# Optimization experiments

Hardware: AMD Instinct MI355X
Metric: run time of the kernel (lower is better)

Reference implementation:

```python
import jax, jax.numpy as jnp
import numpy as np

H = 8          # n_heads
DK = 128       # d_model // h
D = H * DK     # d_model = 1024
B, S = 8, 1024
D_LIST = (32, 64, 96, 128)  # sorted set of hidden//h from config dict


def setup_inputs() -> dict:
    key = jax.random.key(0)
    ks = jax.random.split(key, 13)
    mk = lambda k, shape: jax.random.normal(k, shape, dtype=jnp.float32)
    inp = {
        'query': mk(ks[0], (B, S, D)),
        'key': mk(ks[1], (B, S, D)),
        'value': mk(ks[2], (B, S, D)),
        'config_idx': jax.random.randint(ks[3], (B,), 0, len(D_LIST), dtype=jnp.int32),
        'Wq': mk(ks[4], (D, D)) * 0.02, 'bq': jnp.zeros((D,), jnp.float32),
        'Wk': mk(ks[5], (D, D)) * 0.02, 'bk': jnp.zeros((D,), jnp.float32),
        'Wv': mk(ks[6], (D, D)) * 0.02, 'bv': jnp.zeros((D,), jnp.float32),
        'Wo': mk(ks[7], (D, D)) * 0.02, 'bo': jnp.zeros((D,), jnp.float32),
    }
    return inp


def _mha_arrange(query, key, value, config_idx, Wq, bq, Wk, bk, Wv, bv, Wo, bo):
    Bb, Ss, _ = query.shape
    proj = lambda x, W, b: (x @ W.T + b).reshape(Bb, Ss, H, DK).transpose(0, 2, 1, 3)
    q = proj(query, Wq, bq)   # [B,H,S,DK]
    k = proj(key, Wk, bk)
    v = proj(value, Wv, bv)
    scores = jnp.einsum('bhqd,bhkd->bhqk', q, k) / np.float32(np.sqrt(DK))
    p = jax.nn.softmax(scores, axis=-1)
    ctx = jnp.einsum('bhqk,bhkd->bhqd', p, v).transpose(0, 2, 1, 3)  # [B,S,H,DK]
    # attn_arrange: per-sample width d; pack first d dims of each head densely
    ret = jnp.zeros((Bb, Ss, H * DK), query.dtype)
    for i, d in enumerate(D_LIST):
        packed = ctx[:, :, :, :d].reshape(Bb, Ss, H * d)           # [B,S,H*d]
        packed = jnp.pad(packed, ((0, 0), (0, 0), (0, H * (DK - d))))
        sel = (config_idx == i)[:, None, None]
        ret = ret + jnp.where(sel, packed, jnp.zeros((), query.dtype))
    return ret @ Wo.T + bo


def reference(query, key, value, config_idx, Wq, bq, Wk, bk, Wv, bv, Wo, bo):
    return _mha_arrange(query, key, value, config_idx, Wq, bq, Wk, bk, Wv, bv, Wo, bo)
```

## Files before the change

kernel.cpp:

```cpp
#include <hip/hip_runtime.h>
#include <hip/hip_bf16.h>


typedef __attribute__((ext_vector_type(8))) __bf16 bf16x8;
typedef __attribute__((ext_vector_type(4))) float f32x4;

#define DEV static __device__ __forceinline__

DEV float exp2v(float x) { return __builtin_amdgcn_exp2f(x); }

DEV unsigned short f2bf(float f) {
  union { float f; unsigned int u; } c; c.f = f;
  unsigned int u = c.u + 0x7fffu + ((c.u >> 16) & 1u);
  return (unsigned short)(u >> 16);
}

DEV unsigned cvtpk(float a, float b) {
  unsigned r;
  asm("v_cvt_pk_bf16_f32 %0, %1, %2" : "=v"(r) : "v"(a), "v"(b));
  return r;
}

DEV void gload16(const void* g, void* l) {
  __builtin_amdgcn_global_load_lds((const __attribute__((address_space(1))) void*)g,
                                   (__attribute__((address_space(3))) void*)l, 16, 0, 0);
}

#define LGKM0 do { asm volatile("s_waitcnt lgkmcnt(0)" ::: "memory"); \
                   __builtin_amdgcn_sched_barrier(0); } while (0)
#define BAR   __builtin_amdgcn_s_barrier()
#define VMC4  asm volatile("s_waitcnt vmcnt(4)" ::: "memory")
#define VMC0  asm volatile("s_waitcnt vmcnt(0)" ::: "memory")

DEV void cv4(const float* __restrict__ s, unsigned short* __restrict__ d, int i) {
  const float4 a = *(const float4*)(s + i);
  ushort4 o;
  o.x = f2bf(a.x); o.y = f2bf(a.y); o.z = f2bf(a.z); o.w = f2bf(a.w);
  *(ushort4*)(d + i) = o;
}

__global__ __launch_bounds__(256) void convert_kernel(
    const float* __restrict__ q, const float* __restrict__ k, const float* __restrict__ v,
    const float* __restrict__ wq, const float* __restrict__ wk,
    const float* __restrict__ wv, const float* __restrict__ wo,
    unsigned short* __restrict__ xq, unsigned short* __restrict__ xk,
    unsigned short* __restrict__ xv, unsigned short* __restrict__ wb)
{
  const int i = (blockIdx.x * 256 + threadIdx.x) * 4;
  cv4(q, xq, i);
  cv4(k, xk, i);
  cv4(v, xv, i);
  if (i < 4 * 1024 * 1024) {
    const int which = i >> 20, off = i & 1048575;
    const float* s = which == 0 ? wq : which == 1 ? wk : which == 2 ? wv : wo;
    cv4(s, wb + (which << 20), off);
  }
}

template<int OUTMODE>
__global__ __launch_bounds__(512, 2) void gemm8p(
    const unsigned short* __restrict__ xq, const unsigned short* __restrict__ xk,
    const unsigned short* __restrict__ xv, const unsigned short* __restrict__ wb,
    const float* __restrict__ bq, const float* __restrict__ bk,
    const float* __restrict__ bv,
    unsigned short* __restrict__ Qp, unsigned short* __restrict__ Kp,
    unsigned short* __restrict__ VTp, float* __restrict__ fout)
{
  __shared__ __align__(16) char LDS[131072];
  int z, mt, nt;
  if (OUTMODE == 0) {
    const int swz = ((blockIdx.x & 7) * 48) + (blockIdx.x >> 3);
    z = swz >> 7; const int rem = swz & 127; mt = rem >> 2; nt = rem & 3;
  } else {
    const int swz = ((blockIdx.x & 7) * 16) + (blockIdx.x >> 3);
    z = 0; mt = swz >> 2; nt = swz & 3;
  }
  const int m0 = mt * 256, n0 = nt * 256;
  const unsigned short* Ag = (OUTMODE == 1) ? xq : (z == 0 ? xq : z == 1 ? xk : xv);
  const unsigned short* Bg = (OUTMODE == 1) ? wb : wb + ((size_t)z << 20);
  const float* bias = (OUTMODE == 1) ? bq : (z == 0 ? bq : z == 1 ? bk : bv);

  const int tid = threadIdx.x, lane = tid & 63, w = tid >> 6;
  const int wm = w >> 2, wn = w & 3;
  const int g = lane >> 4, ln = lane & 15;

  const f32x4 fzero = {0.f, 0.f, 0.f, 0.f};
  f32x4 acc[8][4];
#pragma unroll
  for (int i = 0; i < 8; i++)
#pragma unroll
    for (int j = 0; j < 4; j++) acc[i][j] = fzero;

  bf16x8 bfr[4][2];
  bf16x8 afr[2][2];

  auto stageA = [&](int bf, int hf, int k0) {
    const unsigned short* src = Ag + (size_t)(m0 + hf * 128) * 1024 + k0;
    char* base = LDS + bf * 32768 + hf * 16384 + w * 2048;
#pragma unroll
    for (int r2 = 0; r2 < 2; ++r2) {
      const int o = w * 2048 + r2 * 1024 + lane * 16;
      const int rwi = o >> 7, cb = o & 127;
      gload16(src + (size_t)rwi * 1024 + ((cb ^ ((rwi & 7) << 4)) >> 1), base + r2 * 1024);
    }
  };
  auto stageB = [&](int bf, int hf, int k0) {
    const unsigned short* src = Bg + (size_t)(n0 + hf * 128) * 1024 + k0;
    char* base = LDS + 65536 + bf * 32768 + hf * 16384 + w * 2048;
#pragma unroll
    for (int r2 = 0; r2 < 2; ++r2) {
      const int o = w * 2048 + r2 * 1024 + lane * 16;
      const int rwi = o >> 7, cb = o & 127;
      gload16(src + (size_t)rwi * 1024 + ((cb ^ ((rwi & 7) << 4)) >> 1), base + r2 * 1024);
    }
  };
  auto rdA = [&](int bf, int q) {
#pragma unroll
    for (int p = 0; p < 2; ++p)
#pragma unroll
      for (int kc = 0; kc < 2; ++kc) {
        const int rwi = (2 * q + p) * 16 + ln;
        const int cb = (kc * 64 + g * 16) ^ ((rwi & 7) << 4);
        afr[p][kc] = *(const bf16x8*)(LDS + bf * 32768 + wm * 16384 + rwi * 128 + cb);
      }
  };
  auto rdB = [&](int bf) {
#pragma unroll
    for (int nf = 0; nf < 4; ++nf)
#pragma unroll
      for (int kc = 0; kc < 2; ++kc) {
        const int rwi = (wn & 1) * 64 + nf * 16 + ln;
        const int cb = (kc * 64 + g * 16) ^ ((rwi & 7) << 4);
        bfr[nf][kc] = *(const bf16x8*)(LDS + 65536 + bf * 32768 + (wn >> 1) * 16384 + rwi * 128 + cb);
      }
  };
  auto mm = [&](int q) {
    __builtin_amdgcn_s_setprio(1);
#pragma unroll
    for (int p = 0; p < 2; ++p)
#pragma unroll
      for (int nf = 0; nf < 4; ++nf)
#pragma unroll
        for (int kc = 0; kc < 2; ++kc)
          acc[2 * q + p][nf] =
              __builtin_amdgcn_mfma_f32_16x16x32_bf16(afr[p][kc], bfr[nf][kc],
                                                      acc[2 * q + p][nf], 0, 0, 0);
    __builtin_amdgcn_s_setprio(0);
  };

  stageB(0, 0, 0); stageB(0, 1, 0);
  stageA(0, 0, 0); stageA(0, 1, 0);
  stageB(1, 0, 64); stageB(1, 1, 64);
  VMC4; BAR;

  for (int j = 0; j < 8; ++j) {
    const int kO = (2 * j + 1) << 6, kNE = (2 * j + 2) << 6, kNO = (2 * j + 3) << 6;
    const bool pf = j < 7;
    rdB(0); rdA(0, 0); stageA(1, 0, kO);
    LGKM0; BAR; mm(0); BAR;
    rdA(0, 1); stageA(1, 1, kO);
    LGKM0; BAR; mm(1); BAR;
    rdA(0, 2); if (pf) stageB(0, 0, kNE);
    LGKM0; BAR; mm(2); BAR;
    rdA(0, 3); if (pf) stageB(0, 1, kNE);
    LGKM0; BAR; mm(3);
    if (pf) { VMC4; } else { VMC0; }
    BAR;
    rdB(1); rdA(1, 0); if (pf) stageA(0, 0, kNE);
    LGKM0; BAR; mm(0); BAR;
    rdA(1, 1); if (pf) stageA(0, 1, kNE);
    LGKM0; BAR; mm(1); BAR;
    rdA(1, 2); if (pf) stageB(1, 0, kNO);
    LGKM0; BAR; mm(2); BAR;
    rdA(1, 3); if (pf) stageB(1, 1, kNO);
    LGKM0; BAR; mm(3);
    if (pf) { VMC4; }
    BAR;
  }

  const float QS = 0.12751743f;
#pragma unroll
  for (int mf = 0; mf < 8; ++mf)
#pragma unroll
    for (int nf = 0; nf < 4; ++nf) {
      const int m = m0 + wm * 128 + mf * 16 + g * 4;
      const int n = n0 + wn * 64 + nf * 16 + ln;
      const float bn = bias[n];
      if (OUTMODE == 1) {
#pragma unroll
        for (int r = 0; r < 4; ++r)
          fout[(size_t)(m + r) * 1024 + n] = acc[mf][nf][r] + bn;
      } else if (z == 0) {
#pragma unroll
        for (int r = 0; r < 4; ++r)
          Qp[(size_t)(m + r) * 1024 + n] = f2bf((acc[mf][nf][r] + bn) * QS);
      } else if (z == 1) {
#pragma unroll
        for (int r = 0; r < 4; ++r)
          Kp[(size_t)(m + r) * 1024 + n] = f2bf(acc[mf][nf][r] + bn);
      } else {
        const int b = m >> 10, s0 = m & 1023;
        uint2 pk;
        pk.x = cvtpk(acc[mf][nf][0] + bn, acc[mf][nf][1] + bn);
        pk.y = cvtpk(acc[mf][nf][2] + bn, acc[mf][nf][3] + bn);
        *(uint2*)(VTp + (((size_t)(b * 8) << 7 | n) << 10) + s0) = pk;
      }
    }
}

__global__ __launch_bounds__(256) void attn_kernel(
    const unsigned short* __restrict__ Qp, const unsigned short* __restrict__ Kp,
    const unsigned short* __restrict__ VT, const int* __restrict__ cfg,
    unsigned short* __restrict__ ret)
{
  __shared__ __align__(16) unsigned short Ks[2][64 * 128];
  __shared__ __align__(16) unsigned short Vs[2][128 * 64];
  __shared__ __align__(16) unsigned short Ps[4 * 16 * 64];
  const int bx = blockIdx.x;
  const int qb = bx >> 6, bh = bx & 63, b = bh >> 3, h = bh & 7;
  const int tid = threadIdx.x, lane = tid & 63, w = tid >> 6;
  const int g = lane >> 4, ln = lane & 15;
  const int q0 = qb * 64;
  const f32x4 fzero = {0.f, 0.f, 0.f, 0.f};

  bf16x8 qf[4];
  {
    const unsigned short* qrow = Qp + ((size_t)(b * 1024 + q0 + w * 16 + ln)) * 1024 + h * 128;
#pragma unroll
    for (int kc = 0; kc < 4; kc++) qf[kc] = *(const bf16x8*)(qrow + kc * 32 + g * 8);
  }
  float m_run = -1e30f, l_run = 0.f;
  f32x4 o_acc[8];
#pragma unroll
  for (int i = 0; i < 8; i++) o_acc[i] = fzero;

  auto stage = [&](int buf, int kv0) {
#pragma unroll
    for (int i = 0; i < 4; ++i) {
      const int obase = i * 4096 + w * 1024;
      const int o = obase + lane * 16;
      {
        const int r = o >> 8, cb = o & 255;
        const int cs = cb ^ ((r & 7) << 4);
        gload16(Kp + ((size_t)(b * 1024 + kv0 + r)) * 1024 + h * 128 + (cs >> 1),
                (char*)Ks + buf * 16384 + obase);
      }
      {
        const int r = o >> 7, cb = o & 127;
        const int cs = cb ^ ((r & 7) << 4);
        gload16(VT + ((size_t)((b * 8 + h) * 128 + r)) * 1024 + kv0 + (cs >> 1),
                (char*)Vs + buf * 16384 + obase);
      }
    }
  };

  stage(0, 0);
  asm volatile("s_waitcnt vmcnt(0)" ::: "memory");
  __syncthreads();

  int cur = 0;
  for (int t = 0; t < 16; ++t) {
    if (t < 15) stage(cur ^ 1, (t + 1) * 64);

    f32x4 sc[4];
    __builtin_amdgcn_s_setprio(1);
#pragma unroll
    for (int nb = 0; nb < 4; ++nb) {
      sc[nb] = fzero;
      const int rr = nb * 16 + ln;
      const int sw = (rr & 7) << 4;
#pragma unroll
      for (int kc = 0; kc < 4; ++kc) {
        const bf16x8 kf = *(const bf16x8*)((const char*)Ks + cur * 16384 + rr * 256 +
                                           (((kc * 32 + g * 8) << 1) ^ sw));
        sc[nb] = __builtin_amdgcn_mfma_f32_16x16x32_bf16(kf, qf[kc], sc[nb], 0, 0, 0);
      }
    }
    __builtin_amdgcn_s_setprio(0);

    float mnb[4];
#pragma unroll
    for (int nb = 0; nb < 4; ++nb)
      mnb[nb] = fmaxf(fmaxf(sc[nb][0], sc[nb][1]), fmaxf(sc[nb][2], sc[nb][3]));
    float pmax = fmaxf(fmaxf(mnb[0], mnb[1]), fmaxf(mnb[2], mnb[3]));
    pmax = fmaxf(pmax, __shfl_xor(pmax, 16));
    pmax = fmaxf(pmax, __shfl_xor(pmax, 32));
    if (__any(pmax > m_run + 11.5f)) {
      const float mnew = fmaxf(m_run, pmax);
      const float alpha = exp2v(m_run - mnew);
      l_run *= alpha;
      m_run = mnew;
      float ar[4];
#pragma unroll
      for (int r = 0; r < 4; ++r)
        ar[r] = __shfl(alpha, (lane & 48) | (((lane >> 4) & 3) << 2) | r);
#pragma unroll
      for (int i = 0; i < 8; i++)
#pragma unroll
        for (int r = 0; r < 4; r++) o_acc[i][r] *= ar[r];
    }
    float sum = 0.f;
    float pvv[16];
#pragma unroll
    for (int nb = 0; nb < 4; ++nb)
#pragma unroll
      for (int r = 0; r < 4; ++r) {
        const float p = exp2v(sc[nb][r] - m_run);
        pvv[nb * 4 + r] = p; sum += p;
      }
    l_run += sum;

    {
      char* pbase = (char*)Ps + w * 2048 + ln * 128;
#pragma unroll
      for (int nb = 0; nb < 4; ++nb) {
        uint2 pk;
        pk.x = cvtpk(pvv[nb * 4 + 0], pvv[nb * 4 + 1]);
        pk.y = cvtpk(pvv[nb * 4 + 2], pvv[nb * 4 + 3]);
        *(uint2*)(pbase + (((16 * nb + 4 * g) << 1) ^ ((ln & 7) << 4))) = pk;
      }
    }
    bf16x8 pf[2];
#pragma unroll
    for (int kc = 0; kc < 2; kc++)
      pf[kc] = *(const bf16x8*)((const char*)Ps + w * 2048 + ln * 128 +
                                (((kc * 32 + g * 8) << 1) ^ ((ln & 7) << 4)));

    __builtin_amdgcn_s_setprio(1);
#pragma unroll
    for (int nb2 = 0; nb2 < 8; ++nb2) {
      const int rr = nb2 * 16 + ln;
      const int sw = (rr & 7) << 4;
#pragma unroll
      for (int kc = 0; kc < 2; ++kc) {
        const bf16x8 vf = *(const bf16x8*)((const char*)Vs + cur * 16384 + rr * 128 +
                                           (((kc * 32 + g * 8) << 1) ^ sw));
        o_acc[nb2] = __builtin_amdgcn_mfma_f32_16x16x32_bf16(pf[kc], vf, o_acc[nb2], 0, 0, 0);
      }
    }
    __builtin_amdgcn_s_setprio(0);

    if (t < 15) {
      asm volatile("s_waitcnt vmcnt(0)" ::: "memory");
      __syncthreads();
    }
    cur ^= 1;
  }

  l_run += __shfl_xor(l_run, 16);
  l_run += __shfl_xor(l_run, 32);
  float rl[4];
#pragma unroll
  for (int r = 0; r < 4; ++r)
    rl[r] = 1.0f / __shfl(l_run, (lane & 48) | (((lane >> 4) & 3) << 2) | r);
  const int d_b = 32 * (cfg[b] + 1);
  const int zw = 128 - d_b;
  const size_t rowbase = (size_t)(b * 1024 + q0 + w * 16 + g * 4);
#pragma unroll
  for (int nb2 = 0; nb2 < 8; ++nb2) {
    const int dk = nb2 * 16 + ln;
    if (dk < d_b) {
#pragma unroll
      for (int r = 0; r < 4; r++)
        ret[(rowbase + r) * 1024 + h * d_b + dk] = f2bf(o_acc[nb2][r] * rl[r]);
    } else {
#pragma unroll
      for (int r = 0; r < 4; r++)
        ret[(rowbase + r) * 1024 + 8 * d_b + h * zw + (dk - d_b)] = 0;
    }
  }
}

extern "C" void kernel_launch(void* const* d_in, const int* in_sizes, int n_in,
                              void* d_out, int out_size, void* d_ws, size_t ws_size,
                              hipStream_t stream)
{
  (void)in_sizes; (void)n_in; (void)out_size; (void)ws_size;
  const float* q   = (const float*)d_in[0];
  const float* k   = (const float*)d_in[1];
  const float* v   = (const float*)d_in[2];
  const int*   cfg = (const int*)d_in[3];
  const float* Wq  = (const float*)d_in[4];  const float* bq = (const float*)d_in[5];
  const float* Wk  = (const float*)d_in[6];  const float* bk = (const float*)d_in[7];
  const float* Wv  = (const float*)d_in[8];  const float* bv = (const float*)d_in[9];
  const float* Wo  = (const float*)d_in[10]; const float* bo = (const float*)d_in[11];

  const size_t X  = 8192ull * 1024ull;
  const size_t WN = 1024ull * 1024ull;
  char* p = (char*)d_ws;
  unsigned short* xq  = (unsigned short*)p; p += X * 2;
  unsigned short* xk  = (unsigned short*)p; p += X * 2;
  unsigned short* xv  = (unsigned short*)p; p += X * 2;
  unsigned short* wb  = (unsigned short*)p; p += 4 * WN * 2;
  unsigned short* Qp  = (unsigned short*)p; p += X * 2;
  unsigned short* Kp  = (unsigned short*)p; p += X * 2;
  unsigned short* VTp = (unsigned short*)p; p += X * 2;
  unsigned short* ret = (unsigned short*)p; p += X * 2;

  convert_kernel<<<dim3(8192), dim3(256), 0, stream>>>(q, k, v, Wq, Wk, Wv, Wo,
                                                       xq, xk, xv, wb);

  gemm8p<0><<<dim3(384), dim3(512), 0, stream>>>(xq, xk, xv, wb, bq, bk, bv,
                                                 Qp, Kp, VTp, nullptr);

  attn_kernel<<<dim3(1024), dim3(256), 0, stream>>>(Qp, Kp, VTp, cfg, ret);

  gemm8p<1><<<dim3(128), dim3(512), 0, stream>>>(ret, nullptr, nullptr, wb + 3 * WN,
                                                 bo, nullptr, nullptr,
                                                 nullptr, nullptr, nullptr,
                                                 (float*)d_out);
}
```

Baseline: 194.7 us.

## Fuse fp32-to-bf16 activation conversion into QKV GEMM A-tile staging

The separate conversion pass for query/key/value is removed. The QKV GEMM now loads fp32 A tiles into registers, converts them with packed bf16 conversion and writes them to LDS, while weights are still pre-converted. This avoids writing and rereading three bf16 activation copies. The GEMM tile also shrinks from 256x256 to 256x128 with a triple-buffered pipeline and twice as many blocks, at the cost of more register pressure and fp32 global read traffic inside the GEMM.

```diff
diff --git a/kernel.cpp b/kernel.cpp
--- a/kernel.cpp
+++ b/kernel.cpp
@@ -29,8 +29,7 @@
 #define LGKM0 do { asm volatile("s_waitcnt lgkmcnt(0)" ::: "memory"); \
                    __builtin_amdgcn_sched_barrier(0); } while (0)
 #define BAR   __builtin_amdgcn_s_barrier()
-#define VMC4  asm volatile("s_waitcnt vmcnt(4)" ::: "memory")
-#define VMC0  asm volatile("s_waitcnt vmcnt(0)" ::: "memory")
+#define VMC(n) asm volatile("s_waitcnt vmcnt(" #n ")" ::: "memory")
 
 DEV void cv4(const float* __restrict__ s, unsigned short* __restrict__ d, int i) {
   const float4 a = *(const float4*)(s + i);
@@ -39,100 +38,114 @@
   *(ushort4*)(d + i) = o;
 }
 
-__global__ __launch_bounds__(256) void convert_kernel(
-    const float* __restrict__ q, const float* __restrict__ k, const float* __restrict__ v,
+__global__ __launch_bounds__(256) void convert_w(
     const float* __restrict__ wq, const float* __restrict__ wk,
     const float* __restrict__ wv, const float* __restrict__ wo,
-    unsigned short* __restrict__ xq, unsigned short* __restrict__ xk,
-    unsigned short* __restrict__ xv, unsigned short* __restrict__ wb)
+    unsigned short* __restrict__ wb)
 {
   const int i = (blockIdx.x * 256 + threadIdx.x) * 4;
-  cv4(q, xq, i);
-  cv4(k, xk, i);
-  cv4(v, xv, i);
-  if (i < 4 * 1024 * 1024) {
-    const int which = i >> 20, off = i & 1048575;
-    const float* s = which == 0 ? wq : which == 1 ? wk : which == 2 ? wv : wo;
-    cv4(s, wb + (which << 20), off);
-  }
-}
-
-template<int OUTMODE>
-__global__ __launch_bounds__(512, 2) void gemm8p(
-    const unsigned short* __restrict__ xq, const unsigned short* __restrict__ xk,
-    const unsigned short* __restrict__ xv, const unsigned short* __restrict__ wb,
+  const int which = i >> 20, off = i & 1048575;
+  const float* s = which == 0 ? wq : which == 1 ? wk : which == 2 ? wv : wo;
+  cv4(s, wb + (which << 20), off);
+}
+
+template<int AMODE>
+__global__ __launch_bounds__(512, 2) void gemm3b(
+    const float* __restrict__ Aq, const float* __restrict__ Ak,
+    const float* __restrict__ Av, const unsigned short* __restrict__ Abf,
+    const unsigned short* __restrict__ wbase,
     const float* __restrict__ bq, const float* __restrict__ bk,
     const float* __restrict__ bv,
     unsigned short* __restrict__ Qp, unsigned short* __restrict__ Kp,
     unsigned short* __restrict__ VTp, float* __restrict__ fout)
 {
-  __shared__ __align__(16) char LDS[131072];
+  __shared__ __align__(16) char LDS[147456];
   int z, mt, nt;
-  if (OUTMODE == 0) {
-    const int swz = ((blockIdx.x & 7) * 48) + (blockIdx.x >> 3);
-    z = swz >> 7; const int rem = swz & 127; mt = rem >> 2; nt = rem & 3;
+  if (AMODE == 0) {
+    const int swz = (blockIdx.x & 7) * 96 + (blockIdx.x >> 3);
+    z = swz >> 8; const int rem = swz & 255; mt = rem >> 3; nt = rem & 7;
   } else {
-    const int swz = ((blockIdx.x & 7) * 16) + (blockIdx.x >> 3);
-    z = 0; mt = swz >> 2; nt = swz & 3;
-  }
-  const int m0 = mt * 256, n0 = nt * 256;
-  const unsigned short* Ag = (OUTMODE == 1) ? xq : (z == 0 ? xq : z == 1 ? xk : xv);
-  const unsigned short* Bg = (OUTMODE == 1) ? wb : wb + ((size_t)z << 20);
-  const float* bias = (OUTMODE == 1) ? bq : (z == 0 ? bq : z == 1 ? bk : bv);
+    const int swz = (blockIdx.x & 7) * 32 + (blockIdx.x >> 3);
+    z = 0; mt = swz >> 3; nt = swz & 7;
+  }
+  const int m0 = mt * 256, n0 = nt * 128;
+  const float* Af = (AMODE == 0) ? (z == 0 ? Aq : z == 1 ? Ak : Av) : nullptr;
+  const unsigned short* Bg = wbase + ((size_t)(AMODE == 0 ? z : 0) << 20);
+  const float* bias = (AMODE == 0) ? (z == 0 ? bq : z == 1 ? bk : bv) : bq;
 
   const int tid = threadIdx.x, lane = tid & 63, w = tid >> 6;
-  const int wm = w >> 2, wn = w & 3;
+  const int wm = w >> 1, wn = w & 1;
   const int g = lane >> 4, ln = lane & 15;
 
   const f32x4 fzero = {0.f, 0.f, 0.f, 0.f};
-  f32x4 acc[8][4];
-#pragma unroll
-  for (int i = 0; i < 8; i++)
+  f32x4 acc[4][4];
+#pragma unroll
+  for (int i = 0; i < 4; i++)
 #pragma unroll
     for (int j = 0; j < 4; j++) acc[i][j] = fzero;
 
-  bf16x8 bfr[4][2];
-  bf16x8 afr[2][2];
-
-  auto stageA = [&](int bf, int hf, int k0) {
-    const unsigned short* src = Ag + (size_t)(m0 + hf * 128) * 1024 + k0;
-    char* base = LDS + bf * 32768 + hf * 16384 + w * 2048;
-#pragma unroll
-    for (int r2 = 0; r2 < 2; ++r2) {
-      const int o = w * 2048 + r2 * 1024 + lane * 16;
-      const int rwi = o >> 7, cb = o & 127;
-      gload16(src + (size_t)rwi * 1024 + ((cb ^ ((rwi & 7) << 4)) >> 1), base + r2 * 1024);
-    }
-  };
-  auto stageB = [&](int bf, int hf, int k0) {
-    const unsigned short* src = Bg + (size_t)(n0 + hf * 128) * 1024 + k0;
-    char* base = LDS + 65536 + bf * 32768 + hf * 16384 + w * 2048;
-#pragma unroll
-    for (int r2 = 0; r2 < 2; ++r2) {
-      const int o = w * 2048 + r2 * 1024 + lane * 16;
-      const int rwi = o >> 7, cb = o & 127;
-      gload16(src + (size_t)rwi * 1024 + ((cb ^ ((rwi & 7) << 4)) >> 1), base + r2 * 1024);
-    }
-  };
-  auto rdA = [&](int bf, int q) {
-#pragma unroll
-    for (int p = 0; p < 2; ++p)
-#pragma unroll
-      for (int kc = 0; kc < 2; ++kc) {
-        const int rwi = (2 * q + p) * 16 + ln;
-        const int cb = (kc * 64 + g * 16) ^ ((rwi & 7) << 4);
-        afr[p][kc] = *(const bf16x8*)(LDS + bf * 32768 + wm * 16384 + rwi * 128 + cb);
-      }
-  };
-  auto rdB = [&](int bf) {
-#pragma unroll
-    for (int nf = 0; nf < 4; ++nf)
-#pragma unroll
-      for (int kc = 0; kc < 2; ++kc) {
-        const int rwi = (wn & 1) * 64 + nf * 16 + ln;
-        const int cb = (kc * 64 + g * 16) ^ ((rwi & 7) << 4);
-        bfr[nf][kc] = *(const bf16x8*)(LDS + 65536 + bf * 32768 + (wn >> 1) * 16384 + rwi * 128 + cb);
-      }
+  bf16x8 afr[2][2], bfr[4][2];
+
+  auto SB = [&](int buf, int k0) {
+    char* base = LDS + 98304 + buf * 16384 + w * 2048;
+#pragma unroll
+    for (int j2 = 0; j2 < 2; ++j2) {
+      const int o = w * 2048 + j2 * 1024 + lane * 16;
+      const int row = o >> 7, cb = o & 127;
+      gload16(Bg + (size_t)(n0 + row) * 1024 + k0 + ((cb ^ ((row & 7) << 4)) >> 1),
+              base + j2 * 1024);
+    }
+  };
+  auto SA = [&](int buf, int hf, int k0) {
+    char* base = LDS + buf * 32768 + hf * 16384 + w * 2048;
+#pragma unroll
+    for (int j2 = 0; j2 < 2; ++j2) {
+      const int o = w * 2048 + j2 * 1024 + lane * 16;
+      const int row = o >> 7, cb = o & 127;
+      gload16(Abf + (size_t)(m0 + hf * 128 + row) * 1024 + k0 + ((cb ^ ((row & 7) << 4)) >> 1),
+              base + j2 * 1024);
+    }
+  };
+
+  const int arow = tid >> 2;
+  const int acol = (tid & 3) << 4;
+  const int wsw = (arow & 7) << 4;
+  const int wc0 = ((tid & 3) * 32) ^ wsw;
+  const int wc1 = ((tid & 3) * 32 + 16) ^ wsw;
+
+#define LA4(d0, d1, d2, d3, hf, k0) do { \
+    const float* _s = Af + (size_t)(m0 + (hf) * 128 + arow) * 1024 + (k0) + acol; \
+    d0 = *(const float4*)(_s); d1 = *(const float4*)(_s + 4); \
+    d2 = *(const float4*)(_s + 8); d3 = *(const float4*)(_s + 12); } while (0)
+
+#define WA4(buf, hf, s0, s1, s2, s3) do { \
+    char* _d = LDS + (buf) * 32768 + (hf) * 16384 + arow * 128; \
+    uint4 _p0, _p1; \
+    _p0.x = cvtpk(s0.x, s0.y); _p0.y = cvtpk(s0.z, s0.w); \
+    _p0.z = cvtpk(s1.x, s1.y); _p0.w = cvtpk(s1.z, s1.w); \
+    _p1.x = cvtpk(s2.x, s2.y); _p1.y = cvtpk(s2.z, s2.w); \
+    _p1.z = cvtpk(s3.x, s3.y); _p1.w = cvtpk(s3.z, s3.w); \
+    *(uint4*)(_d + wc0) = _p0; *(uint4*)(_d + wc1) = _p1; } while (0)
+
+  auto rdA = [&](int buf, int q) {
+#pragma unroll
+    for (int p = 0; p < 2; ++p) {
+      const int row = wm * 64 + (2 * q + p) * 16 + ln;
+      const int sw = (row & 7) << 4;
+#pragma unroll
+      for (int kc = 0; kc < 2; ++kc)
+        afr[p][kc] = *(const bf16x8*)(LDS + buf * 32768 + row * 128 + ((kc * 64 + g * 16) ^ sw));
+    }
+  };
+  auto rdB = [&](int buf) {
+#pragma unroll
+    for (int nf = 0; nf < 4; ++nf) {
+      const int row = wn * 64 + nf * 16 + ln;
+      const int sw = (row & 7) << 4;
+#pragma unroll
+      for (int kc = 0; kc < 2; ++kc)
+        bfr[nf][kc] = *(const bf16x8*)(LDS + 98304 + buf * 16384 + row * 128 + ((kc * 64 + g * 16) ^ sw));
+    }
   };
   auto mm = [&](int q) {
     __builtin_amdgcn_s_setprio(1);
@@ -148,62 +161,95 @@
     __builtin_amdgcn_s_setprio(0);
   };
 
-  stageB(0, 0, 0); stageB(0, 1, 0);
-  stageA(0, 0, 0); stageA(0, 1, 0);
-  stageB(1, 0, 64); stageB(1, 1, 64);
-  VMC4; BAR;
-
-  for (int j = 0; j < 8; ++j) {
-    const int kO = (2 * j + 1) << 6, kNE = (2 * j + 2) << 6, kNO = (2 * j + 3) << 6;
-    const bool pf = j < 7;
-    rdB(0); rdA(0, 0); stageA(1, 0, kO);
-    LGKM0; BAR; mm(0); BAR;
-    rdA(0, 1); stageA(1, 1, kO);
-    LGKM0; BAR; mm(1); BAR;
-    rdA(0, 2); if (pf) stageB(0, 0, kNE);
-    LGKM0; BAR; mm(2); BAR;
-    rdA(0, 3); if (pf) stageB(0, 1, kNE);
-    LGKM0; BAR; mm(3);
-    if (pf) { VMC4; } else { VMC0; }
-    BAR;
-    rdB(1); rdA(1, 0); if (pf) stageA(0, 0, kNE);
-    LGKM0; BAR; mm(0); BAR;
-    rdA(1, 1); if (pf) stageA(0, 1, kNE);
-    LGKM0; BAR; mm(1); BAR;
-    rdA(1, 2); if (pf) stageB(1, 0, kNO);
-    LGKM0; BAR; mm(2); BAR;
-    rdA(1, 3); if (pf) stageB(1, 1, kNO);
-    LGKM0; BAR; mm(3);
-    if (pf) { VMC4; }
-    BAR;
-  }
+  float4 a00, a01, a02, a03, a04, a05, a06, a07;
+  float4 a10, a11, a12, a13, a14, a15, a16, a17;
+
+  if (AMODE == 0) {
+    LA4(a00, a01, a02, a03, 0, 0);
+    LA4(a04, a05, a06, a07, 1, 0);
+    SB(0, 0);
+    LA4(a10, a11, a12, a13, 0, 64);
+    LA4(a14, a15, a16, a17, 1, 64);
+    SB(1, 64);
+    WA4(0, 0, a00, a01, a02, a03);
+    WA4(0, 1, a04, a05, a06, a07);
+    VMC(10);
+  } else {
+    SA(0, 0, 0); SA(0, 1, 0);
+    SB(0, 0);
+    SA(1, 0, 64); SA(1, 1, 64);
+    SB(1, 64);
+    VMC(6);
+  }
+  LGKM0; BAR;
+
+#define TILE(t, L0, L1, L2, L3, L4, L5, L6, L7, W0, W1, W2, W3, W4, W5, W6, W7, br, bn, bw) \
+  do { \
+    const int _kL = ((t) + 2) << 6; \
+    const bool _ld = (t) < 14, _wr = (t) < 15; \
+     \
+    rdB(br); rdA(br, 0); \
+    if (AMODE == 0) { \
+      if (_ld) LA4(L0, L1, L2, L3, 0, _kL); \
+      if (_wr) WA4(bn, 0, W0, W1, W2, W3); \
+    } else { \
+      if (_ld) SA(bw, 0, _kL); \
+    } \
+    BAR; LGKM0; mm(0); BAR; \
+     \
+    rdA(br, 1); \
+    if (AMODE == 0) { \
+      if (_ld) LA4(L4, L5, L6, L7, 1, _kL); \
+      if (_wr) WA4(bn, 1, W4, W5, W6, W7); \
+    } else { \
+      if (_ld) SA(bw, 1, _kL); \
+    } \
+    if (_ld) SB(bw, _kL); \
+    BAR; LGKM0; mm(1); \
+    if (_ld) { if (AMODE == 0) VMC(10); else VMC(6); } \
+    else if ((t) < 15) VMC(0); \
+    BAR; \
+  } while (0)
+
+  int br = 0, bn = 1, bw = 2;
+  for (int t2 = 0; t2 < 16; t2 += 2) {
+    TILE(t2, a00, a01, a02, a03, a04, a05, a06, a07,
+             a10, a11, a12, a13, a14, a15, a16, a17, br, bn, bw);
+    { const int x = br; br = bn; bn = bw; bw = x; }
+    TILE(t2 + 1, a10, a11, a12, a13, a14, a15, a16, a17,
+                 a00, a01, a02, a03, a04, a05, a06, a07, br, bn, bw);
+    { const int x = br; br = bn; bn = bw; bw = x; }
+  }
+#undef TILE
+#undef LA4
+#undef WA4
 
   const float QS = 0.12751743f;
 #pragma unroll
-  for (int mf = 0; mf < 8; ++mf)
+  for (int mf = 0; mf < 4; ++mf)
 #pragma unroll
     for (int nf = 0; nf < 4; ++nf) {
-      const int m = m0 + wm * 128 + mf * 16 + g * 4;
+      const int m = m0 + wm * 64 + mf * 16 + g * 4;
       const int n = n0 + wn * 64 + nf * 16 + ln;
-      const float bn = bias[n];
-      if (OUTMODE == 1) {
+      const float bn_ = bias[n];
+      if (AMODE == 1) {
 #pragma unroll
         for (int r = 0; r < 4; ++r)
-          fout[(size_t)(m + r) * 1024 + n] = acc[mf][nf][r] + bn;
+          fout[(size_t)(m + r) * 1024 + n] = acc[mf][nf][r] + bn_;
       } else if (z == 0) {
 #pragma unroll
         for (int r = 0; r < 4; ++r)
-          Qp[(size_t)(m + r) * 1024 + n] = f2bf((acc[mf][nf][r] + bn) * QS);
+          Qp[(size_t)(m + r) * 1024 + n] = f2bf((acc[mf][nf][r] + bn_) * QS);
       } else if (z == 1) {
 #pragma unroll
         for (int r = 0; r < 4; ++r)
-          Kp[(size_t)(m + r) * 1024 + n] = f2bf(acc[mf][nf][r] + bn);
+          Kp[(size_t)(m + r) * 1024 + n] = f2bf(acc[mf][nf][r] + bn_);
       } else {
         const int b = m >> 10, s0 = m & 1023;
         uint2 pk;
-        pk.x = cvtpk(acc[mf][nf][0] + bn, acc[mf][nf][1] + bn);
-        pk.y = cvtpk(acc[mf][nf][2] + bn, acc[mf][nf][3] + bn);
-        *(uint2*)(VTp + (((size_t)(b * 8) << 7 | n) << 10) + s0) = pk;
+        pk.x = cvtpk(acc[mf][nf][0] + bn_, acc[mf][nf][1] + bn_);
+        pk.y = cvtpk(acc[mf][nf][2] + bn_, acc[mf][nf][3] + bn_);
+        *(uint2*)(VTp + (((size_t)(b * 1024 + n)) << 10) + s0) = pk;
       }
     }
 }
@@ -388,25 +434,21 @@
   const size_t X  = 8192ull * 1024ull;
   const size_t WN = 1024ull * 1024ull;
   char* p = (char*)d_ws;
-  unsigned short* xq  = (unsigned short*)p; p += X * 2;
-  unsigned short* xk  = (unsigned short*)p; p += X * 2;
-  unsigned short* xv  = (unsigned short*)p; p += X * 2;
   unsigned short* wb  = (unsigned short*)p; p += 4 * WN * 2;
   unsigned short* Qp  = (unsigned short*)p; p += X * 2;
   unsigned short* Kp  = (unsigned short*)p; p += X * 2;
   unsigned short* VTp = (unsigned short*)p; p += X * 2;
   unsigned short* ret = (unsigned short*)p; p += X * 2;
 
-  convert_kernel<<<dim3(8192), dim3(256), 0, stream>>>(q, k, v, Wq, Wk, Wv, Wo,
-                                                       xq, xk, xv, wb);
-
-  gemm8p<0><<<dim3(384), dim3(512), 0, stream>>>(xq, xk, xv, wb, bq, bk, bv,
-                                                 Qp, Kp, VTp, nullptr);
+  convert_w<<<dim3(4096), dim3(256), 0, stream>>>(Wq, Wk, Wv, Wo, wb);
+
+  gemm3b<0><<<dim3(768), dim3(512), 0, stream>>>(q, k, v, nullptr, wb,
+                                                 bq, bk, bv, Qp, Kp, VTp, nullptr);
 
   attn_kernel<<<dim3(1024), dim3(256), 0, stream>>>(Qp, Kp, VTp, cfg, ret);
 
-  gemm8p<1><<<dim3(128), dim3(512), 0, stream>>>(ret, nullptr, nullptr, wb + 3 * WN,
-                                                 bo, nullptr, nullptr,
+  gemm3b<1><<<dim3(256), dim3(512), 0, stream>>>(nullptr, nullptr, nullptr, ret,
+                                                 wb + 3 * WN, bo, nullptr, nullptr,
                                                  nullptr, nullptr, nullptr,
                                                  (float*)d_out);
 }
```

Result: slower. 203.5 us (+4.5%).

## Replace output projection with smaller-tile GEMM and reorder barriers in QKV GEMM

Applied to the files above, without the earlier changes.

The output projection previously reused the 256x256-tile pipelined GEMM with only 128 blocks, which underfills a chip with many CUs. A new simple 128x128-tile kernel launches 512 blocks of 256 threads to raise parallelism, at the cost of no software pipelining (synchronous load then compute each k-step). The QKV GEMM's LDS wait macro drops its sched_barrier, and the wait now sits after the workgroup barrier, which gives the compiler more freedom to schedule the LDS reads against the MFMAs.

```diff
diff --git a/kernel.cpp b/kernel.cpp
--- a/kernel.cpp
+++ b/kernel.cpp
@@ -26,8 +26,7 @@
                                    (__attribute__((address_space(3))) void*)l, 16, 0, 0);
 }
 
-#define LGKM0 do { asm volatile("s_waitcnt lgkmcnt(0)" ::: "memory"); \
-                   __builtin_amdgcn_sched_barrier(0); } while (0)
+#define LGKM0 asm volatile("s_waitcnt lgkmcnt(0)" ::: "memory")
 #define BAR   __builtin_amdgcn_s_barrier()
 #define VMC4  asm volatile("s_waitcnt vmcnt(4)" ::: "memory")
 #define VMC0  asm volatile("s_waitcnt vmcnt(0)" ::: "memory")
@@ -57,28 +56,22 @@
   }
 }
 
-template<int OUTMODE>
 __global__ __launch_bounds__(512, 2) void gemm8p(
     const unsigned short* __restrict__ xq, const unsigned short* __restrict__ xk,
     const unsigned short* __restrict__ xv, const unsigned short* __restrict__ wb,
     const float* __restrict__ bq, const float* __restrict__ bk,
     const float* __restrict__ bv,
     unsigned short* __restrict__ Qp, unsigned short* __restrict__ Kp,
-    unsigned short* __restrict__ VTp, float* __restrict__ fout)
+    unsigned short* __restrict__ VTp)
 {
   __shared__ __align__(16) char LDS[131072];
-  int z, mt, nt;
-  if (OUTMODE == 0) {
-    const int swz = ((blockIdx.x & 7) * 48) + (blockIdx.x >> 3);
-    z = swz >> 7; const int rem = swz & 127; mt = rem >> 2; nt = rem & 3;
-  } else {
-    const int swz = ((blockIdx.x & 7) * 16) + (blockIdx.x >> 3);
-    z = 0; mt = swz >> 2; nt = swz & 3;
-  }
+  const int swz = ((blockIdx.x & 7) * 48) + (blockIdx.x >> 3);
+  const int z = swz >> 7; const int rem = swz & 127;
+  const int mt = rem >> 2, nt = rem & 3;
   const int m0 = mt * 256, n0 = nt * 256;
-  const unsigned short* Ag = (OUTMODE == 1) ? xq : (z == 0 ? xq : z == 1 ? xk : xv);
-  const unsigned short* Bg = (OUTMODE == 1) ? wb : wb + ((size_t)z << 20);
-  const float* bias = (OUTMODE == 1) ? bq : (z == 0 ? bq : z == 1 ? bk : bv);
+  const unsigned short* Ag = z == 0 ? xq : z == 1 ? xk : xv;
+  const unsigned short* Bg = wb + ((size_t)z << 20);
+  const float* bias = z == 0 ? bq : z == 1 ? bk : bv;
 
   const int tid = threadIdx.x, lane = tid & 63, w = tid >> 6;
   const int wm = w >> 2, wn = w & 3;
@@ -157,23 +150,23 @@
     const int kO = (2 * j + 1) << 6, kNE = (2 * j + 2) << 6, kNO = (2 * j + 3) << 6;
     const bool pf = j < 7;
     rdB(0); rdA(0, 0); stageA(1, 0, kO);
-    LGKM0; BAR; mm(0); BAR;
+    BAR; LGKM0; mm(0); BAR;
     rdA(0, 1); stageA(1, 1, kO);
-    LGKM0; BAR; mm(1); BAR;
+    BAR; LGKM0; mm(1); BAR;
     rdA(0, 2); if (pf) stageB(0, 0, kNE);
-    LGKM0; BAR; mm(2); BAR;
+    BAR; LGKM0; mm(2); BAR;
     rdA(0, 3); if (pf) stageB(0, 1, kNE);
-    LGKM0; BAR; mm(3);
+    BAR; LGKM0; mm(3);
     if (pf) { VMC4; } else { VMC0; }
     BAR;
     rdB(1); rdA(1, 0); if (pf) stageA(0, 0, kNE);
-    LGKM0; BAR; mm(0); BAR;
+    BAR; LGKM0; mm(0); BAR;
     rdA(1, 1); if (pf) stageA(0, 1, kNE);
-    LGKM0; BAR; mm(1); BAR;
+    BAR; LGKM0; mm(1); BAR;
     rdA(1, 2); if (pf) stageB(1, 0, kNO);
-    LGKM0; BAR; mm(2); BAR;
+    BAR; LGKM0; mm(2); BAR;
     rdA(1, 3); if (pf) stageB(1, 1, kNO);
-    LGKM0; BAR; mm(3);
+    BAR; LGKM0; mm(3);
     if (pf) { VMC4; }
     BAR;
   }
@@ -186,11 +179,7 @@
       const int m = m0 + wm * 128 + mf * 16 + g * 4;
       const int n = n0 + wn * 64 + nf * 16 + ln;
       const float bn = bias[n];
-      if (OUTMODE == 1) {
-#pragma unroll
-        for (int r = 0; r < 4; ++r)
-          fout[(size_t)(m + r) * 1024 + n] = acc[mf][nf][r] + bn;
-      } else if (z == 0) {
+      if (z == 0) {
 #pragma unroll
         for (int r = 0; r < 4; ++r)
           Qp[(size_t)(m + r) * 1024 + n] = f2bf((acc[mf][nf][r] + bn) * QS);
@@ -205,6 +194,70 @@
         pk.y = cvtpk(acc[mf][nf][2] + bn, acc[mf][nf][3] + bn);
         *(uint2*)(VTp + (((size_t)(b * 8) << 7 | n) << 10) + s0) = pk;
       }
+    }
+}
+
+__global__ __launch_bounds__(256) void gemm_out(
+    const unsigned short* __restrict__ A, const unsigned short* __restrict__ Bt,
+    const float* __restrict__ bias, float* __restrict__ Cout)
+{
+  __shared__ __align__(16) unsigned short As[128 * 64];
+  __shared__ __align__(16) unsigned short Bs[128 * 64];
+  const int bid = blockIdx.x;
+  const int swz = (bid & 7) * 64 + (bid >> 3);
+  const int m0 = (swz >> 3) * 128, n0 = (swz & 7) * 128;
+  const int tid = threadIdx.x;
+  const int lane = tid & 63, w = tid >> 6;
+  const int wr = w >> 1, wc = w & 1;
+  const int g = lane >> 4, ln = lane & 15;
+  const f32x4 fzero = {0.f, 0.f, 0.f, 0.f};
+
+  f32x4 acc[4][4];
+#pragma unroll
+  for (int i = 0; i < 4; i++)
+#pragma unroll
+    for (int j = 0; j < 4; j++) acc[i][j] = fzero;
+
+  for (int k0 = 0; k0 < 1024; k0 += 64) {
+    __syncthreads();
+#pragma unroll
+    for (int i = 0; i < 4; ++i) {
+      const int obase = i * 4096 + w * 1024;
+      const int o = obase + lane * 16;
+      const int r = o >> 7, cb = o & 127;
+      gload16(A  + (size_t)(m0 + r) * 1024 + k0 + (cb >> 1), (char*)As + obase);
+      gload16(Bt + (size_t)(n0 + r) * 1024 + k0 + (cb >> 1), (char*)Bs + obase);
+    }
+    asm volatile("s_waitcnt vmcnt(0)" ::: "memory");
+    __syncthreads();
+#pragma unroll
+    for (int kc = 0; kc < 2; ++kc) {
+      const int ko = kc * 32 + g * 8;
+      bf16x8 af[4], bfr[4];
+#pragma unroll
+      for (int mi = 0; mi < 4; ++mi)
+        af[mi] = *(const bf16x8*)(As + (wr * 64 + mi * 16 + ln) * 64 + ko);
+#pragma unroll
+      for (int ni = 0; ni < 4; ++ni)
+        bfr[ni] = *(const bf16x8*)(Bs + (wc * 64 + ni * 16 + ln) * 64 + ko);
+#pragma unroll
+      for (int mi = 0; mi < 4; ++mi)
+#pragma unroll
+        for (int ni = 0; ni < 4; ++ni)
+          acc[mi][ni] = __builtin_amdgcn_mfma_f32_16x16x32_bf16(af[mi], bfr[ni], acc[mi][ni], 0, 0, 0);
+    }
+  }
+
+#pragma unroll
+  for (int mi = 0; mi < 4; ++mi)
+#pragma unroll
+    for (int ni = 0; ni < 4; ++ni) {
+      const int mb = m0 + wr * 64 + mi * 16 + g * 4;
+      const int n  = n0 + wc * 64 + ni * 16 + ln;
+      const float bn = bias[n];
+#pragma unroll
+      for (int r = 0; r < 4; ++r)
+        Cout[(size_t)(mb + r) * 1024 + n] = acc[mi][ni][r] + bn;
     }
 }
 
@@ -400,13 +453,10 @@
   convert_kernel<<<dim3(8192), dim3(256), 0, stream>>>(q, k, v, Wq, Wk, Wv, Wo,
                                                        xq, xk, xv, wb);
 
-  gemm8p<0><<<dim3(384), dim3(512), 0, stream>>>(xq, xk, xv, wb, bq, bk, bv,
-                                                 Qp, Kp, VTp, nullptr);
+  gemm8p<<<dim3(384), dim3(512), 0, stream>>>(xq, xk, xv, wb, bq, bk, bv,
+                                              Qp, Kp, VTp);
 
   attn_kernel<<<dim3(1024), dim3(256), 0, stream>>>(Qp, Kp, VTp, cfg, ret);
 
-  gemm8p<1><<<dim3(128), dim3(512), 0, stream>>>(ret, nullptr, nullptr, wb + 3 * WN,
-                                                 bo, nullptr, nullptr,
-                                                 nullptr, nullptr, nullptr,
-                                                 (float*)d_out);
-}
+  gemm_out<<<dim3(512), dim3(256), 0, stream>>>(ret, wb + 3 * WN, bo, (float*)d_out);
+}
```

Result: no change. 191.6 us (-1.6%).
